# Optimization experiments

Measured on AMD Instinct MI355X. Metric: run time of the kernel, lower is better.

## Reference

```python
import jax, jax.numpy as jnp
import numpy as np

U10_IDX, V10_IDX = 0, 1
WIND_THRESH = 0.5


def _gru(x, h, Wih, Whh, bih, bhh):
    # standard torch GRUCell math
    gi = x @ Wih.T + bih
    gh = h @ Whh.T + bhh
    ir, iz, inn = jnp.split(gi, 3, axis=-1)
    hr, hz, hnn = jnp.split(gh, 3, axis=-1)
    r = jax.nn.sigmoid(ir + hr)
    z = jax.nn.sigmoid(iz + hz)
    n = jnp.tanh(inn + r * hnn)
    return (1.0 - z) * n + z * h


def setup_inputs() -> dict:
    B, N, H, F, Th, Tf = 256, 184, 128, 8, 24, 24
    key = jax.random.key(0)
    ks = jax.random.split(key, 24)
    s = 0.1
    f32 = jnp.float32
    feature = jax.random.normal(ks[0], (B, Th + Tf, N, F), f32)
    pm25_hist = jax.random.uniform(ks[1], (B, Th, N, 1), dtype=f32)
    adj_mat = (jax.random.uniform(ks[2], (N, N)) < 0.1).astype(f32)
    angles = jax.random.uniform(ks[3], (N, N), f32, 0.0, 2.0 * np.pi)
    C = F + 1  # ChebConv in-channels = in_dim + out_dim
    return dict(
        feature=feature, pm25_hist=pm25_hist, adj_mat=adj_mat, angles=angles,
        W_ih_hist=s * jax.random.normal(ks[4], (3 * H, 2), f32),
        W_hh_hist=s * jax.random.normal(ks[5], (3 * H, H), f32),
        b_ih_hist=s * jax.random.normal(ks[6], (3 * H,), f32),
        b_hh_hist=s * jax.random.normal(ks[7], (3 * H,), f32),
        fc_hist_w=s * jax.random.normal(ks[8], (1, H), f32),
        fc_hist_b=s * jax.random.normal(ks[9], (1,), f32),
        cheb_w0=s * jax.random.normal(ks[10], (C, 1), f32),
        cheb_w1=s * jax.random.normal(ks[11], (C, 1), f32),
        cheb_b=s * jax.random.normal(ks[12], (1,), f32),
        W_ih=s * jax.random.normal(ks[13], (3 * H, C + 1), f32),
        W_hh=s * jax.random.normal(ks[14], (3 * H, H), f32),
        b_ih=s * jax.random.normal(ks[15], (3 * H,), f32),
        b_hh=s * jax.random.normal(ks[16], (3 * H,), f32),
        fc_out_w=s * jax.random.normal(ks[17], (1, H), f32),
        fc_out_b=s * jax.random.normal(ks[18], (1,), f32),
    )


def reference(feature, pm25_hist, adj_mat, angles,
              W_ih_hist, W_hh_hist, b_ih_hist, b_hh_hist,
              fc_hist_w, fc_hist_b,
              cheb_w0, cheb_w1, cheb_b,
              W_ih, W_hh, b_ih, b_hh,
              fc_out_w, fc_out_b):
    B, T, N, F = feature.shape
    H = W_hh.shape[1]
    Th = pm25_hist.shape[1]
    comp1 = jnp.cos(angles)                                # [N,N]
    comp2 = jnp.cos(angles - jnp.float32(np.pi / 2.0))     # [N,N]
    adj_b = adj_mat > 0

    # ---- history GRU over pm25_hist ----
    def hist_step(carry, p):
        hn, xn = carry
        x = jnp.concatenate([xn, p], axis=-1).reshape(B * N, 2)
        hn = _gru(x, hn, W_ih_hist, W_hh_hist, b_ih_hist, b_hh_hist)
        xn = hn.reshape(B, N, H) @ fc_hist_w.T + fc_hist_b
        return (hn, xn), None

    h0 = jnp.zeros((B * N, H), feature.dtype)
    x0 = jnp.zeros((B, N, 1), feature.dtype)
    (hn, xn), _ = jax.lax.scan(hist_step, (h0, x0), jnp.swapaxes(pm25_hist, 0, 1))

    # ---- forecast: dynamic wind-gated graph + ChebConv(K=2) + GRU ----
    def fore_step(carry, f):
        hn, xn = carry
        x = jnp.concatenate([xn, f], axis=-1)              # [B,N,F+1]
        u = f[..., U10_IDX]                                # [B,N]
        v = f[..., V10_IDX]
        wind = u[:, :, None] * comp1[None] + v[:, :, None] * comp2[None]
        # edge i->j iff adj and wind projection >= threshold
        M = jnp.logical_and(wind >= WIND_THRESH, adj_b[None]).astype(x.dtype)
        deg = M.sum(-1)                                    # source degree [B,N]
        has = deg > 0
        dinv = jnp.where(has, 1.0 / jnp.sqrt(jnp.where(has, deg, 1.0)), 0.0)
        # ChebConv scaled Laplacian (lambda_max=2, sym norm):
        # L_hat x [j] = -dinv_j * sum_i dinv_i * M[i,j] * x[i] + (0 if deg_j>0 else -1) * x[j]
        y = jnp.einsum('bij,bic->bjc', M * dinv[:, :, None], x)
        y = -dinv[:, :, None] * y + jnp.where(has, 0.0, -1.0)[:, :, None] * x
        g = jax.nn.sigmoid(x @ cheb_w0 + y @ cheb_w1 + cheb_b)  # [B,N,1]
        x2 = jnp.concatenate([x, g], axis=-1).reshape(B * N, F + 2)
        hn = _gru(x2, hn, W_ih, W_hh, b_ih, b_hh)
        xn = hn.reshape(B, N, H) @ fc_out_w.T + fc_out_b
        return (hn, xn), xn

    fore_feat = jnp.swapaxes(feature[:, Th:], 0, 1)        # [Tf,B,N,F]
    (_, _), preds = jax.lax.scan(fore_step, (hn, xn), fore_feat)
    return jnp.swapaxes(preds, 0, 1)                       # [B,Tf,N,1]
```

## Files before the change

kernel.cpp:

```cpp
#include <hip/hip_runtime.h>
#include <hip/hip_bf16.h>
#include <math.h>

#define BB 256
#define NN 184
#define HH 128
#define FF 8
#define TH 24
#define TF 24
#define KA 160
#define NG 512
#define RPAD 192
#define STRH 136
#define NT 1024
#define NW3 552
#define LOG2E 1.44269504088896f

#define REC_F 8832
#define REC_H 2944
#define OFF_DINV 4416
#define OFF_G 5152
#define OFF_AXF 5888

typedef __attribute__((ext_vector_type(8))) short bf16x8;
typedef __attribute__((ext_vector_type(4))) float f32x4;
typedef __attribute__((ext_vector_type(2))) unsigned u32x2;

__host__ __device__ __forceinline__ long recOff(int b, int t) {
    const long PB = (long)TH * REC_H + (long)TF * REC_F;
    return (long)b * PB + ((t < TH) ? (long)t * REC_H
                                    : (long)TH * REC_H + (long)(t - TH) * REC_F);
}

__device__ __forceinline__ unsigned short f2bf(float f) {
    unsigned u = __float_as_uint(f);
    u += 0x7fffu + ((u >> 16) & 1u);
    return (unsigned short)(u >> 16);
}
__device__ __forceinline__ unsigned pkbf(float a, float b) {
    __hip_bfloat162 h = __float22bfloat162_rn(make_float2(a, b));
    return *reinterpret_cast<unsigned*>(&h);
}
__device__ __forceinline__ void gload16(const void* src, void* dst) {
    __builtin_amdgcn_global_load_lds(
        (const __attribute__((address_space(1))) unsigned int*)src,
        (__attribute__((address_space(3))) unsigned int*)dst, 16, 0, 0);
}

__global__ void prep_weights(const float* __restrict__ WhhH, const float* __restrict__ WihH,
                             const float* __restrict__ WhhF, const float* __restrict__ WihF,
                             const float* __restrict__ bihH, const float* __restrict__ bhhH,
                             const float* __restrict__ bihF, const float* __restrict__ bhhF,
                             unsigned short* __restrict__ WaH, unsigned short* __restrict__ WaF) {
    int idx = blockIdx.x * 256 + threadIdx.x;
    if (idx >= NG * KA) return;
    int jp = idx / KA, k = idx % KA;
    int j = jp & 127, part = jp >> 7;
    float vh = 0.f, vf = 0.f;
    if (part <= 1) {
        int row = part * 128 + j;
        if (k < 128) { vh = WhhH[row * 128 + k]; vf = WhhF[row * 128 + k]; }
        else {
            int s = k - 128;
            if (s == 0)  vh = WihH[row * 2 + 1];
            if (s < 8)   vf = WihF[row * 10 + (s + 1)];
            if (s == 8)  { vh = WihH[row * 2 + 0]; vf = WihF[row * 10 + 0]; }
            if (s == 9)  vf = WihF[row * 10 + 9];
            if (s == 11) { vh = bihH[row] + bhhH[row]; vf = bihF[row] + bhhF[row]; }
        }
    } else if (part == 2) {
        if (k < 128) { vh = WhhH[(256 + j) * 128 + k]; vf = WhhF[(256 + j) * 128 + k]; }
        else if (k == 139) { vh = bhhH[256 + j]; vf = bhhF[256 + j]; }
    } else {
        if (k >= 128) {
            int s = k - 128;
            if (s == 0)  vh = WihH[(256 + j) * 2 + 1];
            if (s < 8)   vf = WihF[(256 + j) * 10 + (s + 1)];
            if (s == 8)  { vh = WihH[(256 + j) * 2 + 0]; vf = WihF[(256 + j) * 10 + 0]; }
            if (s == 9)  vf = WihF[(256 + j) * 10 + 9];
            if (s == 11) { vh = bihH[256 + j]; vf = bihF[256 + j]; }
        }
    }
    float sc = (part <= 1) ? LOG2E : 2.0f * LOG2E;
    WaH[idx] = f2bf(vh * sc);
    WaF[idx] = f2bf(vf * sc);
}

__global__ void prep_edges(const float* __restrict__ angles, const float* __restrict__ adj,
                           float4* __restrict__ edges, int* __restrict__ cnt) {
    int idx = blockIdx.x * 256 + threadIdx.x;
    if (idx < NN * NN && adj[idx] > 0.f) {
        float a = angles[idx];
        int pos = atomicAdd(cnt, 1);
        float4 r;
        r.x = cosf(a);
        r.y = cosf(a - 1.57079632679489662f);
        r.z = __int_as_float(idx / NN);
        r.w = __int_as_float(idx % NN);
        edges[pos] = r;
    }
}

__global__ __launch_bounds__(256) void prep_graph(
    const float* __restrict__ feature, const float* __restrict__ pm25,
    const float4* __restrict__ edges, const int* __restrict__ ecnt,
    const float* __restrict__ cw0, const float* __restrict__ cw1,
    const float* __restrict__ cbb, char* __restrict__ xrec)
{
    const int bt = blockIdx.x;
    const int b = bt / (TH + TF), tt = bt % (TH + TF);
    const int tid = threadIdx.x;
    __shared__ float f8[NN * FF];
    __shared__ unsigned long long mT[NN][3];
    __shared__ int dg[NN];
    __shared__ float di[NN];

    char* rec = xrec + recOff(b, tt);
    if (tt < TH) {
        if (tid < NN) {
            unsigned short pb = f2bf(pm25[((long)b * TH + tt) * NN + tid]);
            unsigned* dst = (unsigned*)rec + tid * 4;
            dst[0] = (unsigned)pb; dst[1] = 0; dst[2] = 0; dst[3] = 0;
        }
        return;
    }

    const float4* fb4 = (const float4*)(feature + ((long)b * (TH + TF) + tt) * (NN * FF));
    for (int i = tid; i < (NN * FF) / 4; i += 256) ((float4*)f8)[i] = fb4[i];
    for (int i = tid; i < NN * 3; i += 256) ((unsigned long long*)mT)[i] = 0ull;
    for (int i = tid; i < NN; i += 256) dg[i] = 0;
    __syncthreads();
    const int nE = *ecnt;
    for (int e = tid; e < nE; e += 256) {
        float4 r = edges[e];
        int ii = __float_as_int(r.z), jj = __float_as_int(r.w);
        if (f8[ii * FF] * r.x + f8[ii * FF + 1] * r.y >= 0.5f) {
            atomicAdd(&dg[ii], 1);
            atomicOr(&mT[jj][ii >> 6], 1ull << (ii & 63));
        }
    }
    __syncthreads();
    if (tid < NN) di[tid] = (dg[tid] > 0) ? rsqrtf((float)dg[tid]) : 0.f;
    __syncthreads();
    unsigned long long* mr = (unsigned long long*)rec;
    for (int i = tid; i < NW3; i += 256) mr[i] = ((const unsigned long long*)mT)[i];
    if (tid < NN) {
        int j = tid;
        float acc[8];
        #pragma unroll
        for (int c = 0; c < 8; ++c) acc[c] = 0.f;
        #pragma unroll
        for (int wd = 0; wd < 3; ++wd) {
            unsigned long long m = mT[j][wd];
            while (m) {
                int bp = __ffsll(m) - 1; m &= m - 1;
                int i = wd * 64 + bp;
                float d = di[i];
                #pragma unroll
                for (int c = 0; c < 8; ++c) acc[c] += d * f8[i * FF + c];
            }
        }
        float dj = di[j];
        float hzj = (dj > 0.f) ? 0.f : -1.f;
        float G = cbb[0];
        #pragma unroll
        for (int c = 0; c < 8; ++c) {
            float xv = f8[j * FF + c];
            float y = -dj * acc[c] + hzj * xv;
            G += xv * cw0[c + 1] + y * cw1[c + 1];
        }
        ((float*)(rec + OFF_DINV))[j] = dj;
        ((float*)(rec + OFF_G))[j] = G;
        unsigned short* ax = (unsigned short*)(rec + OFF_AXF) + j * 8;
        #pragma unroll
        for (int c = 0; c < 8; ++c) ax[c] = f2bf(f8[j * FF + c]);
    }
}

__global__ __launch_bounds__(NT, 4) void fused_dgc(
    const unsigned short* __restrict__ WaH,
    const unsigned short* __restrict__ WaF,
    const float* __restrict__ fchw, const float* __restrict__ fchb,
    const float* __restrict__ fcow, const float* __restrict__ fcob,
    const float* __restrict__ cw0, const float* __restrict__ cw1,
    const char* __restrict__ xrec,
    float* __restrict__ pred)
{
    __shared__ unsigned short Ah[2][RPAD * STRH];
    __shared__ unsigned short AxR[RPAD * 8];
    __shared__ __align__(16) char stg[2][8960];
    __shared__ float red_s[RPAD * 9];
    __shared__ float2 dx_s[NN];
    __shared__ float fcls_f[132];
    __shared__ unsigned short zero16[8];

    const int tid = threadIdx.x;
    const int bb = blockIdx.x;
    const int w = tid >> 6, lane = tid & 63, q = lane >> 4, lq = lane & 15;
    const int cg = w & 7, rh = w >> 3;

    for (int i = tid; i < RPAD * STRH; i += NT) Ah[0][i] = 0;
    for (int i = tid; i < RPAD * 8; i += NT)
        AxR[i] = ((i & 7) == 3) ? (unsigned short)0x3F80 : (unsigned short)0;
    if (tid < 8) zero16[tid] = 0;
    if (tid < NN) dx_s[tid] = make_float2(0.f, 0.f);

    bf16x8 wregH[3][4];
    bf16x8 wregX[4];
    auto load_phase = [&](const unsigned short* Wa, const float* fcw, const float* fcb) {
        const int jcol = cg * 16 + lq;
        #pragma unroll
        for (int g = 0; g < 3; ++g)
            #pragma unroll
            for (int kc = 0; kc < 4; ++kc)
                wregH[g][kc] = *(const bf16x8*)(Wa + (long)(g * 128 + jcol) * KA + kc * 32 + q * 8);
        #pragma unroll
        for (int g = 0; g < 4; ++g)
            wregX[g] = *(const bf16x8*)(Wa + (long)(g * 128 + jcol) * KA + 128 + q * 8);
        if (tid < 132) fcls_f[tid] = (tid < 128) ? fcw[tid] : ((tid == 128) ? fcb[0] : 0.f);
    };
    load_phase(WaH, fchw, fchb);

    if (tid < NN)
        gload16(xrec + recOff(bb, 0) + (long)tid * 16,
                (char*)stg[0] + OFF_AXF + (tid & ~63) * 16);

    const float w00 = cw0[0], w10 = cw1[0];

    float hreg[24];
    #pragma unroll
    for (int i = 0; i < 24; ++i) hreg[i] = 0.f;

    int p = 0;
    __syncthreads();

    for (int t = 0; t < TH + TF; ++t) {
        const unsigned long long* maskS = (const unsigned long long*)stg[p];
        const float* GS = (const float*)(stg[p] + OFF_G);
        const unsigned short* AxFS = (const unsigned short*)(stg[p] + OFF_AXF);

        if (t >= TH) {
            const int jg = tid >> 2, wd = tid & 3;
            if (jg < NN) {
                unsigned long long m = (wd < 3) ? maskS[jg * 3 + wd] : 0ull;
                float acc = 0.f;
                while (m) {
                    int bp = __ffsll(m) - 1; m &= m - 1;
                    float2 dxv = dx_s[wd * 64 + bp];
                    acc += dxv.x * dxv.y;
                }
                acc += __shfl_xor(acc, 1);
                acc += __shfl_xor(acc, 2);
                if (wd == 0) {
                    float2 dxj = dx_s[jg];
                    float hzj = (dxj.x > 0.f) ? 0.f : -1.f;
                    float y0 = -dxj.x * acc + hzj * dxj.y;
                    float pre = GS[jg] + dxj.y * w00 + y0 * w10;
                    float g = __builtin_amdgcn_rcpf(1.0f + exp2f(-LOG2E * pre));
                    AxR[jg * 8 + 1] = f2bf(g);
                }
            }
            __syncthreads();
        }

        const int t2 = t + 1;
        if (t2 < TH + TF) {
            const int nch = (t2 < TH) ? NN : NW3;
            if (tid < nch)
                gload16(xrec + recOff(bb, t2) + (long)tid * 16,
                        (char*)stg[p ^ 1] + ((t2 < TH) ? OFF_AXF : 0) + (tid & ~63) * 16);
        }

        f32x4 fw = *(const f32x4*)&fcls_f[cg * 16 + q * 4];
        #pragma unroll
        for (int rl = 0; rl < 6; ++rl) {
            const int row = rh * 96 + rl * 16 + lq;
            const int ro = row * STRH;
            f32x4 a0 = {0.f,0.f,0.f,0.f}, a1 = {0.f,0.f,0.f,0.f}, a2 = {0.f,0.f,0.f,0.f};
            #pragma unroll
            for (int kc = 0; kc < 4; ++kc) {
                bf16x8 bh = *(const bf16x8*)(&Ah[p][ro + kc * 32 + q * 8]);
                a0 = __builtin_amdgcn_mfma_f32_16x16x32_bf16(wregH[0][kc], bh, a0, 0, 0, 0);
                a1 = __builtin_amdgcn_mfma_f32_16x16x32_bf16(wregH[1][kc], bh, a1, 0, 0, 0);
                a2 = __builtin_amdgcn_mfma_f32_16x16x32_bf16(wregH[2][kc], bh, a2, 0, 0, 0);
            }
            const unsigned short* bxp = (q == 0) ? (AxFS + row * 8)
                                      : (q == 1) ? (AxR + row * 8) : zero16;
            bf16x8 bx = *(const bf16x8*)bxp;
            a0 = __builtin_amdgcn_mfma_f32_16x16x32_bf16(wregX[0], bx, a0, 0, 0, 0);
            a1 = __builtin_amdgcn_mfma_f32_16x16x32_bf16(wregX[1], bx, a1, 0, 0, 0);
            a2 = __builtin_amdgcn_mfma_f32_16x16x32_bf16(wregX[2], bx, a2, 0, 0, 0);
            f32x4 a3 = {0.f,0.f,0.f,0.f};
            a3 = __builtin_amdgcn_mfma_f32_16x16x32_bf16(wregX[3], bx, a3, 0, 0, 0);

            float hn[4];
            #pragma unroll
            for (int rg = 0; rg < 4; ++rg) {
                float rr = __builtin_amdgcn_rcpf(1.0f + exp2f(-a0[rg]));
                float zz = __builtin_amdgcn_rcpf(1.0f + exp2f(-a1[rg]));
                float wv = fmaf(rr, a2[rg], a3[rg]);
                unsigned sg = __float_as_uint(wv) & 0x80000000u;
                float e = exp2f(-fabsf(wv));
                float tv = (1.0f - e) * __builtin_amdgcn_rcpf(1.0f + e);
                tv = __uint_as_float(__float_as_uint(tv) ^ sg);
                float hv = fmaf(zz, hreg[rl * 4 + rg] - tv, tv);
                hreg[rl * 4 + rg] = hv;
                hn[rg] = hv;
            }
            float pf = hn[0] * fw.x + hn[1] * fw.y + hn[2] * fw.z + hn[3] * fw.w;
            pf += __shfl_xor(pf, 16);
            pf += __shfl_xor(pf, 32);
            u32x2 pk;
            pk[0] = pkbf(hn[0], hn[1]);
            pk[1] = pkbf(hn[2], hn[3]);
            *(u32x2*)&Ah[p ^ 1][ro + cg * 16 + q * 4] = pk;
            if (q == 0) red_s[row * 9 + cg] = pf;
        }
        __syncthreads();

        if (tid < NN) {
            float xn = fcls_f[128];
            #pragma unroll
            for (int c = 0; c < 8; ++c) xn += red_s[tid * 9 + c];
            float dv = 0.f;
            if (t2 >= TH && t2 < TH + TF)
                dv = *(const float*)(stg[p ^ 1] + OFF_DINV + tid * 4);
            dx_s[tid] = make_float2(dv, xn);
            AxR[tid * 8 + 0] = f2bf(xn);
            if (t >= TH) pred[((long)bb * TF + (t - TH)) * NN + tid] = xn;
        }
        __syncthreads();

        if (t == TH - 1)
            load_phase(WaF, fcow, fcob);
        p ^= 1;
    }
}

extern "C" void kernel_launch(void* const* d_in, const int* in_sizes, int n_in,
                              void* d_out, int out_size, void* d_ws, size_t ws_size,
                              hipStream_t stream) {
    const float* feature = (const float*)d_in[0];
    const float* pm25    = (const float*)d_in[1];
    const float* adj     = (const float*)d_in[2];
    const float* angles  = (const float*)d_in[3];
    const float* W_ih_h  = (const float*)d_in[4];
    const float* W_hh_h  = (const float*)d_in[5];
    const float* b_ih_h  = (const float*)d_in[6];
    const float* b_hh_h  = (const float*)d_in[7];
    const float* fch_w   = (const float*)d_in[8];
    const float* fch_b   = (const float*)d_in[9];
    const float* cw0     = (const float*)d_in[10];
    const float* cw1     = (const float*)d_in[11];
    const float* cbb     = (const float*)d_in[12];
    const float* W_ih    = (const float*)d_in[13];
    const float* W_hh    = (const float*)d_in[14];
    const float* b_ih    = (const float*)d_in[15];
    const float* b_hh    = (const float*)d_in[16];
    const float* fco_w   = (const float*)d_in[17];
    const float* fco_b   = (const float*)d_in[18];
    float* pred = (float*)d_out;

    char* ws = (char*)d_ws;
    size_t off = 0;
    unsigned short* WaH   = (unsigned short*)(ws + off); off += (size_t)NG * KA * 2;
    unsigned short* WaF   = (unsigned short*)(ws + off); off += (size_t)NG * KA * 2;
    float4*         edges = (float4*)(ws + off);         off += (size_t)NN * NN * 16;
    int*            cnt   = (int*)(ws + off);            off += 16;
    char*           xrec  = (char*)(ws + off);
    off += (size_t)BB * ((size_t)TH * REC_H + (size_t)TF * REC_F);

    hipMemsetAsync(cnt, 0, 16, stream);
    prep_weights<<<(NG * KA + 255) / 256, 256, 0, stream>>>(
        W_hh_h, W_ih_h, W_hh, W_ih, b_ih_h, b_hh_h, b_ih, b_hh, WaH, WaF);
    prep_edges<<<(NN * NN + 255) / 256, 256, 0, stream>>>(angles, adj, edges, cnt);
    prep_graph<<<BB * (TH + TF), 256, 0, stream>>>(
        feature, pm25, edges, cnt, cw0, cw1, cbb, xrec);

    fused_dgc<<<BB, NT, 0, stream>>>(
        WaH, WaF, fch_w, fch_b, fco_w, fco_b, cw0, cw1, xrec, pred);
}
```

Measured before the change: 707.2 us.

## Loop prep_graph per batch with LDS edge cache, pack hidden state as bf16, use K16 MFMA

prep_graph now runs one block per batch instead of one per (batch, time) step. It loops over the forecast steps and caches the edge list in LDS, so edges are not re-read from global memory for every step. The fused kernel keeps the hidden state in registers as packed bf16 rather than fp32, halving its register footprint. This adds rounding to the recurrent state. The input projection uses a 16x16x16 MFMA when available instead of the 16x16x32 one, which was half zero-padded. The prep launch shrinks to 256 blocks, which may under-fill the GPU.

```diff
diff --git a/kernel.cpp b/kernel.cpp
--- a/kernel.cpp
+++ b/kernel.cpp
@@ -14,6 +14,7 @@
 #define STRH 136
 #define NT 1024
 #define NW3 552
+#define EMAX 4096
 #define LOG2E 1.44269504088896f
 
 #define REC_F 8832
@@ -23,8 +24,15 @@
 #define OFF_AXF 5888
 
 typedef __attribute__((ext_vector_type(8))) short bf16x8;
+typedef __attribute__((ext_vector_type(4))) short bf16x4;
 typedef __attribute__((ext_vector_type(4))) float f32x4;
 typedef __attribute__((ext_vector_type(2))) unsigned u32x2;
+
+#if __has_builtin(__builtin_amdgcn_mfma_f32_16x16x16bf16_1k)
+#define XK16 1
+#else
+#define XK16 0
+#endif
 
 __host__ __device__ __forceinline__ long recOff(int b, int t) {
     const long PB = (long)TH * REC_H + (long)TF * REC_F;
@@ -107,73 +115,82 @@
     const float* __restrict__ cw0, const float* __restrict__ cw1,
     const float* __restrict__ cbb, char* __restrict__ xrec)
 {
-    const int bt = blockIdx.x;
-    const int b = bt / (TH + TF), tt = bt % (TH + TF);
+    const int b = blockIdx.x;
     const int tid = threadIdx.x;
+    __shared__ float4 eL[EMAX];
     __shared__ float f8[NN * FF];
     __shared__ unsigned long long mT[NN][3];
     __shared__ int dg[NN];
     __shared__ float di[NN];
 
-    char* rec = xrec + recOff(b, tt);
-    if (tt < TH) {
+    for (int it = tid; it < TH * NN; it += 256) {
+        int tt = it / NN, j = it - tt * NN;
+        unsigned short pb = f2bf(pm25[((long)b * TH + tt) * NN + j]);
+        uint4* dst = (uint4*)(xrec + recOff(b, tt)) + j;
+        *dst = make_uint4((unsigned)pb, 0u, 0u, 0u);
+    }
+
+    const int nEfull = *ecnt;
+    const int nEL = (nEfull < EMAX) ? nEfull : EMAX;
+    for (int e = tid; e < nEL; e += 256) eL[e] = edges[e];
+
+    float w0c[8], w1c[8];
+    #pragma unroll
+    for (int c = 0; c < 8; ++c) { w0c[c] = cw0[c + 1]; w1c[c] = cw1[c + 1]; }
+    const float cb = cbb[0];
+
+    for (int tt = TH; tt < TH + TF; ++tt) {
+        char* rec = xrec + recOff(b, tt);
+        const float4* fb4 = (const float4*)(feature + ((long)b * (TH + TF) + tt) * (NN * FF));
+        __syncthreads();
+        for (int i = tid; i < (NN * FF) / 4; i += 256) ((float4*)f8)[i] = fb4[i];
+        for (int i = tid; i < NN * 3; i += 256) ((unsigned long long*)mT)[i] = 0ull;
+        for (int i = tid; i < NN; i += 256) dg[i] = 0;
+        __syncthreads();
+        for (int e = tid; e < nEfull; e += 256) {
+            float4 r = (e < nEL) ? eL[e] : edges[e];
+            int ii = __float_as_int(r.z), jj = __float_as_int(r.w);
+            if (f8[ii * FF] * r.x + f8[ii * FF + 1] * r.y >= 0.5f) {
+                atomicAdd(&dg[ii], 1);
+                atomicOr(&mT[jj][ii >> 6], 1ull << (ii & 63));
+            }
+        }
+        __syncthreads();
+        if (tid < NN) di[tid] = (dg[tid] > 0) ? rsqrtf((float)dg[tid]) : 0.f;
+        __syncthreads();
+        unsigned long long* mr = (unsigned long long*)rec;
+        for (int i = tid; i < NW3; i += 256) mr[i] = ((const unsigned long long*)mT)[i];
         if (tid < NN) {
-            unsigned short pb = f2bf(pm25[((long)b * TH + tt) * NN + tid]);
-            unsigned* dst = (unsigned*)rec + tid * 4;
-            dst[0] = (unsigned)pb; dst[1] = 0; dst[2] = 0; dst[3] = 0;
-        }
-        return;
-    }
-
-    const float4* fb4 = (const float4*)(feature + ((long)b * (TH + TF) + tt) * (NN * FF));
-    for (int i = tid; i < (NN * FF) / 4; i += 256) ((float4*)f8)[i] = fb4[i];
-    for (int i = tid; i < NN * 3; i += 256) ((unsigned long long*)mT)[i] = 0ull;
-    for (int i = tid; i < NN; i += 256) dg[i] = 0;
-    __syncthreads();
-    const int nE = *ecnt;
-    for (int e = tid; e < nE; e += 256) {
-        float4 r = edges[e];
-        int ii = __float_as_int(r.z), jj = __float_as_int(r.w);
-        if (f8[ii * FF] * r.x + f8[ii * FF + 1] * r.y >= 0.5f) {
-            atomicAdd(&dg[ii], 1);
-            atomicOr(&mT[jj][ii >> 6], 1ull << (ii & 63));
-        }
-    }
-    __syncthreads();
-    if (tid < NN) di[tid] = (dg[tid] > 0) ? rsqrtf((float)dg[tid]) : 0.f;
-    __syncthreads();
-    unsigned long long* mr = (unsigned long long*)rec;
-    for (int i = tid; i < NW3; i += 256) mr[i] = ((const unsigned long long*)mT)[i];
-    if (tid < NN) {
-        int j = tid;
-        float acc[8];
-        #pragma unroll
-        for (int c = 0; c < 8; ++c) acc[c] = 0.f;
-        #pragma unroll
-        for (int wd = 0; wd < 3; ++wd) {
-            unsigned long long m = mT[j][wd];
-            while (m) {
-                int bp = __ffsll(m) - 1; m &= m - 1;
-                int i = wd * 64 + bp;
-                float d = di[i];
-                #pragma unroll
-                for (int c = 0; c < 8; ++c) acc[c] += d * f8[i * FF + c];
-            }
-        }
-        float dj = di[j];
-        float hzj = (dj > 0.f) ? 0.f : -1.f;
-        float G = cbb[0];
-        #pragma unroll
-        for (int c = 0; c < 8; ++c) {
-            float xv = f8[j * FF + c];
-            float y = -dj * acc[c] + hzj * xv;
-            G += xv * cw0[c + 1] + y * cw1[c + 1];
-        }
-        ((float*)(rec + OFF_DINV))[j] = dj;
-        ((float*)(rec + OFF_G))[j] = G;
-        unsigned short* ax = (unsigned short*)(rec + OFF_AXF) + j * 8;
-        #pragma unroll
-        for (int c = 0; c < 8; ++c) ax[c] = f2bf(f8[j * FF + c]);
+            int j = tid;
+            float acc[8];
+            #pragma unroll
+            for (int c = 0; c < 8; ++c) acc[c] = 0.f;
+            #pragma unroll
+            for (int wd = 0; wd < 3; ++wd) {
+                unsigned long long m = mT[j][wd];
+                while (m) {
+                    int bp = __ffsll(m) - 1; m &= m - 1;
+                    int i = wd * 64 + bp;
+                    float d = di[i];
+                    #pragma unroll
+                    for (int c = 0; c < 8; ++c) acc[c] += d * f8[i * FF + c];
+                }
+            }
+            float dj = di[j];
+            float hzj = (dj > 0.f) ? 0.f : -1.f;
+            float G = cb;
+            #pragma unroll
+            for (int c = 0; c < 8; ++c) {
+                float xv = f8[j * FF + c];
+                float y = -dj * acc[c] + hzj * xv;
+                G += xv * w0c[c] + y * w1c[c];
+            }
+            ((float*)(rec + OFF_DINV))[j] = dj;
+            ((float*)(rec + OFF_G))[j] = G;
+            unsigned short* ax = (unsigned short*)(rec + OFF_AXF) + j * 8;
+            #pragma unroll
+            for (int c = 0; c < 8; ++c) ax[c] = f2bf(f8[j * FF + c]);
+        }
     }
 }
 
@@ -206,7 +223,11 @@
     if (tid < NN) dx_s[tid] = make_float2(0.f, 0.f);
 
     bf16x8 wregH[3][4];
+#if XK16
+    bf16x4 wregX[4];
+#else
     bf16x8 wregX[4];
+#endif
     auto load_phase = [&](const unsigned short* Wa, const float* fcw, const float* fcb) {
         const int jcol = cg * 16 + lq;
         #pragma unroll
@@ -216,7 +237,11 @@
                 wregH[g][kc] = *(const bf16x8*)(Wa + (long)(g * 128 + jcol) * KA + kc * 32 + q * 8);
         #pragma unroll
         for (int g = 0; g < 4; ++g)
+#if XK16
+            wregX[g] = *(const bf16x4*)(Wa + (long)(g * 128 + jcol) * KA + 128 + q * 4);
+#else
             wregX[g] = *(const bf16x8*)(Wa + (long)(g * 128 + jcol) * KA + 128 + q * 8);
+#endif
         if (tid < 132) fcls_f[tid] = (tid < 128) ? fcw[tid] : ((tid == 128) ? fcb[0] : 0.f);
     };
     load_phase(WaH, fchw, fchb);
@@ -227,9 +252,9 @@
 
     const float w00 = cw0[0], w10 = cw1[0];
 
-    float hreg[24];
+    unsigned hpk[12];
     #pragma unroll
-    for (int i = 0; i < 24; ++i) hreg[i] = 0.f;
+    for (int i = 0; i < 12; ++i) hpk[i] = 0u;
 
     int p = 0;
     __syncthreads();
@@ -284,18 +309,32 @@
                 a1 = __builtin_amdgcn_mfma_f32_16x16x32_bf16(wregH[1][kc], bh, a1, 0, 0, 0);
                 a2 = __builtin_amdgcn_mfma_f32_16x16x32_bf16(wregH[2][kc], bh, a2, 0, 0, 0);
             }
+            f32x4 a3 = {0.f,0.f,0.f,0.f};
+#if XK16
+            const unsigned short* bxp = (q < 2) ? (AxFS + row * 8 + q * 4)
+                                      : (q == 2) ? (AxR + row * 8) : zero16;
+            bf16x4 bx = *(const bf16x4*)bxp;
+            a0 = __builtin_amdgcn_mfma_f32_16x16x16bf16_1k(wregX[0], bx, a0, 0, 0, 0);
+            a1 = __builtin_amdgcn_mfma_f32_16x16x16bf16_1k(wregX[1], bx, a1, 0, 0, 0);
+            a2 = __builtin_amdgcn_mfma_f32_16x16x16bf16_1k(wregX[2], bx, a2, 0, 0, 0);
+            a3 = __builtin_amdgcn_mfma_f32_16x16x16bf16_1k(wregX[3], bx, a3, 0, 0, 0);
+#else
             const unsigned short* bxp = (q == 0) ? (AxFS + row * 8)
                                       : (q == 1) ? (AxR + row * 8) : zero16;
             bf16x8 bx = *(const bf16x8*)bxp;
             a0 = __builtin_amdgcn_mfma_f32_16x16x32_bf16(wregX[0], bx, a0, 0, 0, 0);
             a1 = __builtin_amdgcn_mfma_f32_16x16x32_bf16(wregX[1], bx, a1, 0, 0, 0);
             a2 = __builtin_amdgcn_mfma_f32_16x16x32_bf16(wregX[2], bx, a2, 0, 0, 0);
-            f32x4 a3 = {0.f,0.f,0.f,0.f};
             a3 = __builtin_amdgcn_mfma_f32_16x16x32_bf16(wregX[3], bx, a3, 0, 0, 0);
+#endif
 
             float hn[4];
+            unsigned hp0 = hpk[rl * 2 + 0], hp1 = hpk[rl * 2 + 1];
             #pragma unroll
             for (int rg = 0; rg < 4; ++rg) {
+                unsigned hu = (rg < 2) ? hp0 : hp1;
+                float ho = ((rg & 1) == 0) ? __uint_as_float(hu << 16)
+                                           : __uint_as_float(hu & 0xffff0000u);
                 float rr = __builtin_amdgcn_rcpf(1.0f + exp2f(-a0[rg]));
                 float zz = __builtin_amdgcn_rcpf(1.0f + exp2f(-a1[rg]));
                 float wv = fmaf(rr, a2[rg], a3[rg]);
@@ -303,16 +342,15 @@
                 float e = exp2f(-fabsf(wv));
                 float tv = (1.0f - e) * __builtin_amdgcn_rcpf(1.0f + e);
                 tv = __uint_as_float(__float_as_uint(tv) ^ sg);
-                float hv = fmaf(zz, hreg[rl * 4 + rg] - tv, tv);
-                hreg[rl * 4 + rg] = hv;
-                hn[rg] = hv;
-            }
+                hn[rg] = fmaf(zz, ho - tv, tv);
+            }
+            unsigned pk0 = pkbf(hn[0], hn[1]), pk1 = pkbf(hn[2], hn[3]);
+            hpk[rl * 2 + 0] = pk0; hpk[rl * 2 + 1] = pk1;
             float pf = hn[0] * fw.x + hn[1] * fw.y + hn[2] * fw.z + hn[3] * fw.w;
             pf += __shfl_xor(pf, 16);
             pf += __shfl_xor(pf, 32);
             u32x2 pk;
-            pk[0] = pkbf(hn[0], hn[1]);
-            pk[1] = pkbf(hn[2], hn[3]);
+            pk[0] = pk0; pk[1] = pk1;
             *(u32x2*)&Ah[p ^ 1][ro + cg * 16 + q * 4] = pk;
             if (q == 0) red_s[row * 9 + cg] = pf;
         }
@@ -374,7 +412,7 @@
     prep_weights<<<(NG * KA + 255) / 256, 256, 0, stream>>>(
         W_hh_h, W_ih_h, W_hh, W_ih, b_ih_h, b_hh_h, b_ih, b_hh, WaH, WaF);
     prep_edges<<<(NN * NN + 255) / 256, 256, 0, stream>>>(angles, adj, edges, cnt);
-    prep_graph<<<BB * (TH + TF), 256, 0, stream>>>(
+    prep_graph<<<BB, 256, 0, stream>>>(
         feature, pm25, edges, cnt, cw0, cw1, cbb, xrec);
 
     fused_dgc<<<BB, NT, 0, stream>>>(
```

Measured after the change: 768.3 us. +8.7%, slower.

## Drop fp32 hidden registers, use K16 MFMA for input, parallelize graph prep

Applied to the files above, without the earlier changes.

Three changes. The main recurrent kernel no longer keeps the fp32 hidden state in 24 registers and instead rereads the previous bf16 hidden state from LDS, which lowers register pressure at the cost of bf16 rounding in the recurrence. The input-projection MFMA is switched to the 16x16x16 bf16 variant so no lanes are wasted on zero padding. The graph-prep kernel splits each node's masked neighbour sum across three threads, one per 64-bit mask word, and reduces through shared memory. Prep also returns earlier for history timesteps and writes one 16-byte store instead of four.

```diff
diff --git a/kernel.cpp b/kernel.cpp
--- a/kernel.cpp
+++ b/kernel.cpp
@@ -23,8 +23,15 @@
 #define OFF_AXF 5888
 
 typedef __attribute__((ext_vector_type(8))) short bf16x8;
+typedef __attribute__((ext_vector_type(4))) short bf16x4;
 typedef __attribute__((ext_vector_type(4))) float f32x4;
 typedef __attribute__((ext_vector_type(2))) unsigned u32x2;
+
+#if __has_builtin(__builtin_amdgcn_mfma_f32_16x16x16bf16_1k)
+#define XK16 1
+#else
+#define XK16 0
+#endif
 
 __host__ __device__ __forceinline__ long recOff(int b, int t) {
     const long PB = (long)TH * REC_H + (long)TF * REC_F;
@@ -110,20 +117,22 @@
     const int bt = blockIdx.x;
     const int b = bt / (TH + TF), tt = bt % (TH + TF);
     const int tid = threadIdx.x;
+
+    char* rec = xrec + recOff(b, tt);
+    if (tt < TH) {
+        if (tid < NN) {
+            unsigned short pb = f2bf(pm25[((long)b * TH + tt) * NN + tid]);
+            uint4* dst = (uint4*)rec + tid;
+            *dst = make_uint4((unsigned)pb, 0u, 0u, 0u);
+        }
+        return;
+    }
+
     __shared__ float f8[NN * FF];
     __shared__ unsigned long long mT[NN][3];
     __shared__ int dg[NN];
     __shared__ float di[NN];
-
-    char* rec = xrec + recOff(b, tt);
-    if (tt < TH) {
-        if (tid < NN) {
-            unsigned short pb = f2bf(pm25[((long)b * TH + tt) * NN + tid]);
-            unsigned* dst = (unsigned*)rec + tid * 4;
-            dst[0] = (unsigned)pb; dst[1] = 0; dst[2] = 0; dst[3] = 0;
-        }
-        return;
-    }
+    __shared__ float red[NW3][8];
 
     const float4* fb4 = (const float4*)(feature + ((long)b * (TH + TF) + tt) * (NN * FF));
     for (int i = tid; i < (NN * FF) / 4; i += 256) ((float4*)f8)[i] = fb4[i];
@@ -144,29 +153,33 @@
     __syncthreads();
     unsigned long long* mr = (unsigned long long*)rec;
     for (int i = tid; i < NW3; i += 256) mr[i] = ((const unsigned long long*)mT)[i];
+    for (int task = tid; task < NW3; task += 256) {
+        int j = task / 3, wd = task - j * 3;
+        unsigned long long m = mT[j][wd];
+        float acc[8];
+        #pragma unroll
+        for (int c = 0; c < 8; ++c) acc[c] = 0.f;
+        while (m) {
+            int bp = __ffsll(m) - 1; m &= m - 1;
+            int i = wd * 64 + bp;
+            float d = di[i];
+            #pragma unroll
+            for (int c = 0; c < 8; ++c) acc[c] += d * f8[i * FF + c];
+        }
+        #pragma unroll
+        for (int c = 0; c < 8; ++c) red[task][c] = acc[c];
+    }
+    __syncthreads();
     if (tid < NN) {
         int j = tid;
-        float acc[8];
-        #pragma unroll
-        for (int c = 0; c < 8; ++c) acc[c] = 0.f;
-        #pragma unroll
-        for (int wd = 0; wd < 3; ++wd) {
-            unsigned long long m = mT[j][wd];
-            while (m) {
-                int bp = __ffsll(m) - 1; m &= m - 1;
-                int i = wd * 64 + bp;
-                float d = di[i];
-                #pragma unroll
-                for (int c = 0; c < 8; ++c) acc[c] += d * f8[i * FF + c];
-            }
-        }
         float dj = di[j];
         float hzj = (dj > 0.f) ? 0.f : -1.f;
         float G = cbb[0];
         #pragma unroll
         for (int c = 0; c < 8; ++c) {
+            float accc = red[j * 3 + 0][c] + red[j * 3 + 1][c] + red[j * 3 + 2][c];
             float xv = f8[j * FF + c];
-            float y = -dj * acc[c] + hzj * xv;
+            float y = -dj * accc + hzj * xv;
             G += xv * cw0[c + 1] + y * cw1[c + 1];
         }
         ((float*)(rec + OFF_DINV))[j] = dj;
@@ -206,7 +219,11 @@
     if (tid < NN) dx_s[tid] = make_float2(0.f, 0.f);
 
     bf16x8 wregH[3][4];
+#if XK16
+    bf16x4 wregX[4];
+#else
     bf16x8 wregX[4];
+#endif
     auto load_phase = [&](const unsigned short* Wa, const float* fcw, const float* fcb) {
         const int jcol = cg * 16 + lq;
         #pragma unroll
@@ -216,7 +233,11 @@
                 wregH[g][kc] = *(const bf16x8*)(Wa + (long)(g * 128 + jcol) * KA + kc * 32 + q * 8);
         #pragma unroll
         for (int g = 0; g < 4; ++g)
+#if XK16
+            wregX[g] = *(const bf16x4*)(Wa + (long)(g * 128 + jcol) * KA + 128 + q * 4);
+#else
             wregX[g] = *(const bf16x8*)(Wa + (long)(g * 128 + jcol) * KA + 128 + q * 8);
+#endif
         if (tid < 132) fcls_f[tid] = (tid < 128) ? fcw[tid] : ((tid == 128) ? fcb[0] : 0.f);
     };
     load_phase(WaH, fchw, fchb);
@@ -226,10 +247,6 @@
                 (char*)stg[0] + OFF_AXF + (tid & ~63) * 16);
 
     const float w00 = cw0[0], w10 = cw1[0];
-
-    float hreg[24];
-    #pragma unroll
-    for (int i = 0; i < 24; ++i) hreg[i] = 0.f;
 
     int p = 0;
     __syncthreads();
@@ -284,18 +301,33 @@
                 a1 = __builtin_amdgcn_mfma_f32_16x16x32_bf16(wregH[1][kc], bh, a1, 0, 0, 0);
                 a2 = __builtin_amdgcn_mfma_f32_16x16x32_bf16(wregH[2][kc], bh, a2, 0, 0, 0);
             }
+            f32x4 a3 = {0.f,0.f,0.f,0.f};
+#if XK16
+            const unsigned short* bxp = (q < 2) ? (AxFS + row * 8 + q * 4)
+                                      : (q == 2) ? (AxR + row * 8) : zero16;
+            bf16x4 bx = *(const bf16x4*)bxp;
+            a0 = __builtin_amdgcn_mfma_f32_16x16x16bf16_1k(wregX[0], bx, a0, 0, 0, 0);
+            a1 = __builtin_amdgcn_mfma_f32_16x16x16bf16_1k(wregX[1], bx, a1, 0, 0, 0);
+            a2 = __builtin_amdgcn_mfma_f32_16x16x16bf16_1k(wregX[2], bx, a2, 0, 0, 0);
+            a3 = __builtin_amdgcn_mfma_f32_16x16x16bf16_1k(wregX[3], bx, a3, 0, 0, 0);
+#else
             const unsigned short* bxp = (q == 0) ? (AxFS + row * 8)
                                       : (q == 1) ? (AxR + row * 8) : zero16;
             bf16x8 bx = *(const bf16x8*)bxp;
             a0 = __builtin_amdgcn_mfma_f32_16x16x32_bf16(wregX[0], bx, a0, 0, 0, 0);
             a1 = __builtin_amdgcn_mfma_f32_16x16x32_bf16(wregX[1], bx, a1, 0, 0, 0);
             a2 = __builtin_amdgcn_mfma_f32_16x16x32_bf16(wregX[2], bx, a2, 0, 0, 0);
-            f32x4 a3 = {0.f,0.f,0.f,0.f};
             a3 = __builtin_amdgcn_mfma_f32_16x16x32_bf16(wregX[3], bx, a3, 0, 0, 0);
+#endif
+
+            u32x2 hold = *(const u32x2*)&Ah[p][ro + cg * 16 + q * 4];
 
             float hn[4];
             #pragma unroll
             for (int rg = 0; rg < 4; ++rg) {
+                unsigned hu = hold[rg >> 1];
+                float ho = ((rg & 1) == 0) ? __uint_as_float(hu << 16)
+                                           : __uint_as_float(hu & 0xffff0000u);
                 float rr = __builtin_amdgcn_rcpf(1.0f + exp2f(-a0[rg]));
                 float zz = __builtin_amdgcn_rcpf(1.0f + exp2f(-a1[rg]));
                 float wv = fmaf(rr, a2[rg], a3[rg]);
@@ -303,9 +335,7 @@
                 float e = exp2f(-fabsf(wv));
                 float tv = (1.0f - e) * __builtin_amdgcn_rcpf(1.0f + e);
                 tv = __uint_as_float(__float_as_uint(tv) ^ sg);
-                float hv = fmaf(zz, hreg[rl * 4 + rg] - tv, tv);
-                hreg[rl * 4 + rg] = hv;
-                hn[rg] = hv;
+                hn[rg] = fmaf(zz, ho - tv, tv);
             }
             float pf = hn[0] * fw.x + hn[1] * fw.y + hn[2] * fw.z + hn[3] * fw.w;
             pf += __shfl_xor(pf, 16);
```

After: 691.7 us. 1.02x faster.
